# Optimization experiments

Hardware: AMD Instinct MI355X
Metric: run time of the kernel (lower is better)

Reference implementation:

```python
import jax, jax.numpy as jnp
import numpy as np

B, N, NB, P = 4, 2048, 10, 5
BIG = 1.0e5  # fill value for non-positive gt grasps


def _build_grasps(approach, base, contacts, thickness):
    # approach/base/contacts: [B,N,3], thickness: [B,N] -> [B,N,4,4]
    cross = jnp.cross(approach, base)
    R = jnp.stack([base, cross, approach], axis=-1)            # columns: [base, cross, approach]
    t = contacts + thickness[..., None] * 0.5 * base           # [B,N,3]
    top = jnp.concatenate([R, t[..., None]], axis=-1)          # [B,N,3,4]
    bottom = jnp.broadcast_to(jnp.array([0.0, 0.0, 0.0, 1.0], top.dtype),
                              top.shape[:-2] + (1, 4))
    return jnp.concatenate([top, bottom], axis=-2)             # [B,N,4,4]


def _transform_cps(cp_h, grasps):
    # cp_h: [P,4], grasps: [B,N,4,4] -> transformed control points [B,N,P,3]
    # torch: matmul(control_points, grasps^T)[..., :3]
    return jnp.einsum('pk,bnjk->bnpj', cp_h, grasps)[..., :3]


def _pairwise_sq(a, b):
    # a: [B,Na,P,3], b: [B,Nb,P,3] -> [B,Na,Nb] = sum_{p,c} (a-b)^2
    af = a.reshape(a.shape[0], a.shape[1], -1)
    bf = b.reshape(b.shape[0], b.shape[1], -1)
    a2 = jnp.sum(af * af, axis=-1)
    b2 = jnp.sum(bf * bf, axis=-1)
    d = a2[:, :, None] + b2[:, None, :] - 2.0 * jnp.einsum('bnd,bmd->bnm', af, bf)
    return jnp.maximum(d, 0.0)


def _forward(grasp_dir_head, approach_dir_head, grasp_offset_head, pred_points,
             binary_score_pred, binary_score_head, dir_labels_pc_cam, offset_labels_pc,
             grasp_success_labels_pc, approach_labels_pc_cam, bin_vals, bin_weights,
             control_pts, sym_control_pts):
    succ = grasp_success_labels_pc                              # [B,N] in {0,1}
    pos_in_view = jnp.maximum(jnp.sum(succ, axis=1), 1.0)       # min_geom_loss_divisor = 1.0

    # bin_offsets=True: lookup bin value of argmax bin
    thickness_pred = bin_vals[jnp.argmax(grasp_offset_head, axis=2)]   # [B,N]
    thickness_gt = bin_vals[jnp.argmax(offset_labels_pc, axis=2)]      # [B,N]

    pred_grasps = _build_grasps(approach_dir_head, grasp_dir_head, pred_points, thickness_pred)
    gt_grasps = _build_grasps(approach_labels_pc_cam, dir_labels_pc_cam, pred_points, thickness_gt)
    mask4 = succ.astype(bool)[:, :, None, None]
    pos_gt_grasps = jnp.where(mask4, gt_grasps, jnp.full_like(gt_grasps, BIG))

    ones_col = jnp.ones((P, 1), dtype=control_pts.dtype)
    cp_h = jnp.concatenate([control_pts, ones_col], axis=1)      # [P,4]
    scp_h = jnp.concatenate([sym_control_pts, ones_col], axis=1)

    pred_cp = _transform_cps(cp_h, pred_grasps)                  # [B,N,P,3]
    gt_cp_pos = _transform_cps(cp_h, pos_gt_grasps)
    sym_gt_cp_pos = _transform_cps(scp_h, pos_gt_grasps)

    # pred -> gt ADD-S (top-k with k=1 == min over concat of the two [B,N,N])
    d1 = _pairwise_sq(pred_cp, gt_cp_pos)
    d2 = _pairwise_sq(pred_cp, sym_gt_cp_pos)
    best = jnp.min(jnp.minimum(d1, d2), axis=2)                  # [B,N]
    gate = jnp.minimum(jnp.sum(succ, axis=1, keepdims=True), 1.0)
    min_adds = gate * jnp.sqrt(best)
    adds_loss = jnp.mean(binary_score_pred[:, :, 0] * min_adds)

    # gt -> pred ADD-S with unmasked gt grasps + confidence gather
    gt_cp = _transform_cps(cp_h, gt_grasps)
    sym_gt_cp = _transform_cps(scp_h, gt_grasps)
    dg1 = _pairwise_sq(gt_cp, pred_cp)                           # [B,Ngt,Npred]
    dg2 = _pairwise_sq(sym_gt_cp, pred_cp)
    m1 = jnp.min(dg1, axis=2); i1 = jnp.argmin(dg1, axis=2)
    m2 = jnp.min(dg2, axis=2); i2 = jnp.argmin(dg2, axis=2)
    # torch: where(-m1 < -m2, sym_idcs, idcs) == pick sym when m2 < m1
    idcs = jnp.where(m2 < m1, i2, i1)                            # [B,N]
    min_g2p = jnp.minimum(m1, m2) * succ
    conf = jnp.take_along_axis(binary_score_pred[:, :, 0], idcs, axis=1)
    adds_loss_gt2pred = jnp.mean(jnp.sum(conf * min_g2p, axis=1) / pos_in_view)

    # direction cosine loss
    cos_d = 1.0 - jnp.sum(dir_labels_pc_cam * grasp_dir_head, axis=2)
    dir_cosine_loss = jnp.mean(jnp.sum(cos_d * succ, axis=1) / pos_in_view)

    # approach cosine loss against orthogonalized label
    proj = jnp.sum(grasp_dir_head * approach_labels_pc_cam, axis=2, keepdims=True)
    orthog = approach_labels_pc_cam - proj * grasp_dir_head
    orthog = orthog / jnp.maximum(jnp.linalg.norm(orthog, axis=2, keepdims=True), 1e-12)
    cos_a = 1.0 - jnp.sum(orthog * approach_dir_head, axis=2)
    approach_cosine_loss = jnp.mean(jnp.sum(cos_a * succ, axis=1) / pos_in_view)

    # per-bin sigmoid BCE offset loss, bin-weighted
    bce = (offset_labels_pc * jax.nn.softplus(-grasp_offset_head)
           + (1.0 - offset_labels_pc) * jax.nn.softplus(grasp_offset_head))
    off = jnp.mean(bin_weights[None, None, :] * bce, axis=2)
    offset_loss = jnp.mean(jnp.sum(off * succ, axis=1) / pos_in_view)

    # binary success score BCE
    s = succ[:, :, None]
    score_bce = (s * jax.nn.softplus(-binary_score_head)
                 + (1.0 - s) * jax.nn.softplus(binary_score_head))
    bin_ce_loss = jnp.mean(score_bce)

    total = (1.0 * dir_cosine_loss + 1.0 * bin_ce_loss + 1.0 * offset_loss
             + 1.0 * approach_cosine_loss + 10.0 * adds_loss + 1.0 * adds_loss_gt2pred)
    return total


def setup_inputs():
    key = jax.random.key(0)
    ks = jax.random.split(key, 14)
    unit = lambda x: x / jnp.linalg.norm(x, axis=-1, keepdims=True)
    grasp_dir_head = unit(jax.random.normal(ks[0], (B, N, 3), jnp.float32))
    approach_dir_head = unit(jax.random.normal(ks[1], (B, N, 3), jnp.float32))
    grasp_offset_head = jax.random.normal(ks[2], (B, N, NB), jnp.float32)
    pred_points = jax.random.normal(ks[3], (B, N, 3), jnp.float32) * 0.3
    binary_score_pred = jax.random.uniform(ks[4], (B, N, 1), jnp.float32)
    binary_score_head = jax.random.normal(ks[5], (B, N, 1), jnp.float32)
    dir_labels_pc_cam = unit(jax.random.normal(ks[6], (B, N, 3), jnp.float32))
    offset_labels_pc = jax.nn.one_hot(jax.random.randint(ks[7], (B, N), 0, NB), NB, dtype=jnp.float32)
    grasp_success_labels_pc = jnp.round(jax.random.uniform(ks[8], (B, N), jnp.float32))
    approach_labels_pc_cam = unit(jax.random.normal(ks[9], (B, N, 3), jnp.float32))
    bin_vals = jnp.sort(jax.random.uniform(ks[10], (NB,), jnp.float32) * 0.075)
    bin_weights = jax.random.uniform(ks[11], (NB,), jnp.float32) + 0.5
    control_pts = jax.random.normal(ks[12], (P, 3), jnp.float32) * 0.05
    sym_control_pts = control_pts[jnp.array([0, 1, 3, 2, 4])]  # finger-swapped (symmetric) gripper
    return {
        'grasp_dir_head': grasp_dir_head,
        'approach_dir_head': approach_dir_head,
        'grasp_offset_head': grasp_offset_head,
        'pred_points': pred_points,
        'binary_score_pred': binary_score_pred,
        'binary_score_head': binary_score_head,
        'dir_labels_pc_cam': dir_labels_pc_cam,
        'offset_labels_pc': offset_labels_pc,
        'grasp_success_labels_pc': grasp_success_labels_pc,
        'approach_labels_pc_cam': approach_labels_pc_cam,
        'bin_vals': bin_vals,
        'bin_weights': bin_weights,
        'control_pts': control_pts,
        'sym_control_pts': sym_control_pts,
    }


def reference(grasp_dir_head, approach_dir_head, grasp_offset_head, pred_points,
              binary_score_pred, binary_score_head, dir_labels_pc_cam, offset_labels_pc,
              grasp_success_labels_pc, approach_labels_pc_cam, bin_vals, bin_weights,
              control_pts, sym_control_pts):
    return _forward(grasp_dir_head, approach_dir_head, grasp_offset_head, pred_points,
                    binary_score_pred, binary_score_head, dir_labels_pc_cam, offset_labels_pc,
                    grasp_success_labels_pc, approach_labels_pc_cam, bin_vals, bin_weights,
                    control_pts, sym_control_pts)
```

## Files before the change

### kernel.cpp

```cpp
#include <hip/hip_runtime.h>

#define Bn 4
#define Nn 2048
#define NBn 10
#define BN (Bn*Nn)
#define TCOLS 256
#define NCH 64
#define BIGM 1e32f

#define OFF_PRED 0
#define OFF_GT   (BN*16)
#define OFF_PN2  (2*BN*16)
#define OFF_GN2  (OFF_PN2 + BN)
#define OFF_BEST (OFF_GN2 + BN)
#define OFF_PK   (OFF_BEST + BN)
#define OFF_PART (OFF_PK + BN)

__device__ inline float sp_(float x) {
  return fmaxf(x, 0.0f) + log1pf(expf(-fabsf(x)));
}

__device__ inline float waveMin_(float v) {
  const int INFI = 0x7F800000;
#define DPPMIN(ctrl) \
  v = fminf(v, __int_as_float(__builtin_amdgcn_update_dpp(INFI, __float_as_int(v), ctrl, 0xf, 0xf, false)))
  DPPMIN(0x111);
  DPPMIN(0x112);
  DPPMIN(0x114);
  DPPMIN(0x118);
  DPPMIN(0x142);
  DPPMIN(0x143);
#undef DPPMIN
  return v;
}

__device__ inline float blockSum_(float v, float* red) {
  #pragma unroll
  for (int o = 32; o > 0; o >>= 1) v += __shfl_down(v, o, 64);
  __syncthreads();
  if ((threadIdx.x & 63) == 0) red[threadIdx.x >> 6] = v;
  __syncthreads();
  return red[0] + red[1] + red[2] + red[3];
}

__global__ __launch_bounds__(256) void k_prep(
    const float* __restrict__ gdir, const float* __restrict__ adirp,
    const float* __restrict__ goff, const float* __restrict__ ppts,
    const float* __restrict__ bsh,
    const float* __restrict__ dlab, const float* __restrict__ olab,
    const float* __restrict__ succ, const float* __restrict__ alab,
    const float* __restrict__ binv, const float* __restrict__ binw,
    const float* __restrict__ cpts, const float* __restrict__ scpts,
    float* __restrict__ ws)
{
  __shared__ float red[4];
  const int pb = blockIdx.x;
  const int idx = pb * 256 + threadIdx.x;

  const float gd0=gdir[idx*3+0],  gd1=gdir[idx*3+1],  gd2=gdir[idx*3+2];
  const float ad0=adirp[idx*3+0], ad1=adirp[idx*3+1], ad2=adirp[idx*3+2];
  const float dl0=dlab[idx*3+0],  dl1=dlab[idx*3+1],  dl2=dlab[idx*3+2];
  const float al0=alab[idx*3+0],  al1=alab[idx*3+1],  al2=alab[idx*3+2];
  const float pt0=ppts[idx*3+0],  pt1=ppts[idx*3+1],  pt2=ppts[idx*3+2];
  const float sc = succ[idx];

  float bv = goff[idx*NBn]; int ap = 0;
  #pragma unroll
  for (int k = 1; k < NBn; k++) { float v = goff[idx*NBn+k]; if (v > bv) { bv = v; ap = k; } }
  float bg = olab[idx*NBn]; int ag = 0;
  #pragma unroll
  for (int k = 1; k < NBn; k++) { float v = olab[idx*NBn+k]; if (v > bg) { bg = v; ag = k; } }
  const float tp = binv[ap] * 0.5f;
  const float tg = binv[ag] * 0.5f;

  const float cp0 = ad1*gd2 - ad2*gd1, cp1 = ad2*gd0 - ad0*gd2, cp2 = ad0*gd1 - ad1*gd0;
  const float cg0 = al1*dl2 - al2*dl1, cg1 = al2*dl0 - al0*dl2, cg2 = al0*dl1 - al1*dl0;
  const float tpx = pt0 + tp*gd0, tpy = pt1 + tp*gd1, tpz = pt2 + tp*gd2;
  const float tgx = pt0 + tg*dl0, tgy = pt1 + tg*dl1, tgz = pt2 + tg*dl2;

  float pcp[15], gcp[15];
  float pn2 = 0.f, gn2 = 0.f;
  #pragma unroll
  for (int p = 0; p < 5; p++) {
    const float cx = cpts[p*3], cy = cpts[p*3+1], cz = cpts[p*3+2];
    float x, y, z;
    x = gd0*cx + cp0*cy + ad0*cz + tpx;
    y = gd1*cx + cp1*cy + ad1*cz + tpy;
    z = gd2*cx + cp2*cy + ad2*cz + tpz;
    pcp[p*3+0]=x; pcp[p*3+1]=y; pcp[p*3+2]=z;
    pn2 = fmaf(x,x, fmaf(y,y, fmaf(z,z, pn2)));
    x = dl0*cx + cg0*cy + al0*cz + tgx;
    y = dl1*cx + cg1*cy + al1*cz + tgy;
    z = dl2*cx + cg2*cy + al2*cz + tgz;
    gcp[p*3+0]=x; gcp[p*3+1]=y; gcp[p*3+2]=z;
    gn2 = fmaf(x,x, fmaf(y,y, fmaf(z,z, gn2)));
  }

  float4* pd = (float4*)(ws + OFF_PRED) + (size_t)idx*4;
  pd[0]=make_float4(pcp[0],pcp[1],pcp[2],pcp[3]);
  pd[1]=make_float4(pcp[4],pcp[5],pcp[6],pcp[7]);
  pd[2]=make_float4(pcp[8],pcp[9],pcp[10],pcp[11]);
  pd[3]=make_float4(pcp[12],pcp[13],pcp[14],0.f);
  float4* gdst = (float4*)(ws + OFF_GT) + (size_t)idx*4;
  gdst[0]=make_float4(gcp[0],gcp[1],gcp[2],gcp[3]);
  gdst[1]=make_float4(gcp[4],gcp[5],gcp[6],gcp[7]);
  gdst[2]=make_float4(gcp[8],gcp[9],gcp[10],gcp[11]);
  gdst[3]=make_float4(gcp[12],gcp[13],gcp[14],0.f);
  ws[OFF_PN2+idx] = pn2; ws[OFF_GN2+idx] = gn2;

  ((unsigned*)ws)[OFF_BEST + idx] = 0x7F800000u;
  ((unsigned*)ws)[OFF_PK   + idx] = 0xFFFFFFFFu;

  const float cosd = 1.f - (dl0*gd0 + dl1*gd1 + dl2*gd2);
  const float proj = gd0*al0 + gd1*al1 + gd2*al2;
  const float o0 = al0 - proj*gd0, o1 = al1 - proj*gd1, o2 = al2 - proj*gd2;
  const float on = sqrtf(o0*o0 + o1*o1 + o2*o2);
  const float inv = 1.f / fmaxf(on, 1e-12f);
  const float cosa = 1.f - inv*(o0*ad0 + o1*ad1 + o2*ad2);

  float offv = 0.f;
  #pragma unroll
  for (int k = 0; k < NBn; k++) {
    const float x = goff[idx*NBn+k], lab = olab[idx*NBn+k];
    const float bce = lab * sp_(-x) + (1.f - lab) * sp_(x);
    offv = fmaf(binw[k], bce, offv);
  }
  offv *= (1.0f / NBn);
  const float sb = bsh[idx];
  const float sbce = sc * sp_(-sb) + (1.f - sc) * sp_(sb);

  float* part = ws + OFF_PART + (size_t)pb*8;
  float t;
  t = blockSum_(cosd*sc, red); if (threadIdx.x == 0) part[0] = t;
  t = blockSum_(cosa*sc, red); if (threadIdx.x == 0) part[1] = t;
  t = blockSum_(offv*sc, red); if (threadIdx.x == 0) part[2] = t;
  t = blockSum_(sc, red);      if (threadIdx.x == 0) part[3] = t;
  t = blockSum_(sbce, red);    if (threadIdx.x == 0) part[4] = t;
}

__global__ __launch_bounds__(256, 2) void k_pair(const float* __restrict__ succ,
                                                 float* __restrict__ ws) {
  __shared__ float pls[NCH*16];
  __shared__ float pn2s[NCH];
  __shared__ unsigned bkey[TCOLS];
  const int tile = blockIdx.x * TCOLS, b = blockIdx.z;
  const int bN = b * Nn;
  const int ny0 = blockIdx.y * NCH;
  const int tid = threadIdx.x;
  const int lane = tid & 63;
  const int wid = __builtin_amdgcn_readfirstlane(tid >> 6);

  {
    const int row = tid >> 2, q = tid & 3;
    ((float4*)pls)[tid] = ((const float4*)(ws + OFF_PRED))[(size_t)(bN + ny0 + row)*4 + q];
    if (tid < NCH) pn2s[tid] = ws[OFF_PN2 + bN + ny0 + tid];
    bkey[tid] = 0xFFFFFFFFu;
  }

  float4 gq[4][4];
  float  gnc[4], biasc[4], ex[4], ey[4], ez[4];
  unsigned kk[4];
  const float4* G = (const float4*)(ws + OFF_GT);
  #pragma unroll
  for (int c = 0; c < 4; c++) {
    const int r = bN + tile + c*64 + lane;
    gq[c][0] = G[(size_t)r*4+0]; gq[c][1] = G[(size_t)r*4+1];
    gq[c][2] = G[(size_t)r*4+2]; gq[c][3] = G[(size_t)r*4+3];
    gnc[c]   = ws[OFF_GN2 + r];
    biasc[c] = (succ[r] != 0.f) ? 0.f : BIGM;
    ex[c] = gq[c][2].y - gq[c][1].z;
    ey[c] = gq[c][2].z - gq[c][1].w;
    ez[c] = gq[c][2].w - gq[c][2].x;
    kk[c] = 0xFFFFFFFFu;
  }

  float f[16];
  __syncthreads();

  const float4* PL = (const float4*)pls + (size_t)wid*16*4;

  #pragma unroll
  for (int j = 0; j < 16; j++) {
    const float4 p0 = PL[j*4+0], p1 = PL[j*4+1], p2 = PL[j*4+2], p3 = PL[j*4+3];
    const float pn2 = pn2s[wid*16 + j];
    const float pd0 = p1.z - p2.y, pd1 = p1.w - p2.z, pd2 = p2.x - p2.w;
    const unsigned nl = (unsigned)(ny0 + wid*16 + j), nh = nl | 0x800u;

    float fj = BIGM * 2.f;
    #pragma unroll
    for (int c = 0; c < 4; c++) {
      float s;
      s = fmaf(p0.w, gq[c][0].w, fmaf(p0.z, gq[c][0].z, fmaf(p0.y, gq[c][0].y, p0.x*gq[c][0].x)));
      s = fmaf(p1.w, gq[c][1].w, fmaf(p1.z, gq[c][1].z, fmaf(p1.y, gq[c][1].y, fmaf(p1.x, gq[c][1].x, s))));
      s = fmaf(p2.w, gq[c][2].w, fmaf(p2.z, gq[c][2].z, fmaf(p2.y, gq[c][2].y, fmaf(p2.x, gq[c][2].x, s))));
      const float dot = fmaf(p3.z, gq[c][3].z, fmaf(p3.y, gq[c][3].y, fmaf(p3.x, gq[c][3].x, s)));
      const float del = fmaf(pd0, ex[c], fmaf(pd1, ey[c], pd2*ez[c]));
      const float q1  = fmaf(-2.f, dot, pn2 + gnc[c]);
      const float d1  = fmaxf(q1, 0.f);
      const float d2  = fmaxf(fmaf(-2.f, del, q1), 0.f);

      kk[c] = min(kk[c], min((__float_as_uint(d1) & 0xFFFFF000u) | nl,
                             (__float_as_uint(d2) & 0xFFFFF000u) | nh));

      fj = fminf(fj, fminf(d1, d2) + biasc[c]);
    }
    f[j] = fj;
  }

  #pragma unroll
  for (int j = 0; j < 16; j++) f[j] = waveMin_(f[j]);
  if (lane == 63) {
    #pragma unroll
    for (int j = 0; j < 16; j++)
      atomicMin((unsigned*)ws + OFF_BEST + bN + ny0 + wid*16 + j, __float_as_uint(f[j]));
  }

  #pragma unroll
  for (int c = 0; c < 4; c++) atomicMin(&bkey[c*64 + lane], kk[c]);
  __syncthreads();
  atomicMin((unsigned*)ws + OFF_PK + bN + tile + tid, bkey[tid]);
}

__global__ __launch_bounds__(256) void k_red(const float* __restrict__ bsp,
                                             const float* __restrict__ succ,
                                             float* __restrict__ ws) {
  __shared__ float red[4];
  const int b = blockIdx.y, nt = blockIdx.x;
  const int idx = b*Nn + nt*256 + threadIdx.x;

  const float best = __uint_as_float(((const unsigned*)ws)[OFF_BEST + idx]);
  const float adds = (best < 1e30f) ? bsp[idx] * sqrtf(best) : 0.f;

  const unsigned key = ((const unsigned*)ws)[OFF_PK + idx];
  const float d = __uint_as_float(key & 0xFFFFF000u);
  const int  id = (int)(key & 0x7FFu);
  const float g2p = bsp[b*Nn + id] * d * succ[idx];

  float* part = ws + OFF_PART + (size_t)(b*8 + nt)*8;
  float t;
  t = blockSum_(adds, red); if (threadIdx.x == 0) part[5] = t;
  t = blockSum_(g2p, red);  if (threadIdx.x == 0) part[6] = t;
}

__global__ __launch_bounds__(64) void k_fin(const float* __restrict__ ws, float* __restrict__ out) {
  const int t = threadIdx.x;
  float v[7];
  #pragma unroll
  for (int c = 0; c < 7; c++) v[c] = (t < 32) ? ws[OFF_PART + t*8 + c] : 0.f;
  #pragma unroll
  for (int o = 1; o < 8; o <<= 1) {
    #pragma unroll
    for (int c = 0; c < 7; c++) v[c] += __shfl_xor(v[c], o, 64);
  }
  const float pos = fmaxf(v[3], 1.f);
  float vb   = (v[0] + v[1] + v[2] + v[6]) / pos;
  float bce  = v[4];
  float adds = v[5];
  #pragma unroll
  for (int o = 8; o < 32; o <<= 1) {
    vb   += __shfl_xor(vb,   o, 64);
    bce  += __shfl_xor(bce,  o, 64);
    adds += __shfl_xor(adds, o, 64);
  }
  if (t == 0)
    out[0] = vb * 0.25f + bce * (1.f/BN) + 10.f * adds * (1.f/BN);
}

extern "C" void kernel_launch(void* const* d_in, const int* in_sizes, int n_in,
                              void* d_out, int out_size, void* d_ws, size_t ws_size,
                              hipStream_t stream) {
  const float* gdir  = (const float*)d_in[0];
  const float* adirp = (const float*)d_in[1];
  const float* goff  = (const float*)d_in[2];
  const float* ppts  = (const float*)d_in[3];
  const float* bsp   = (const float*)d_in[4];
  const float* bsh   = (const float*)d_in[5];
  const float* dlab  = (const float*)d_in[6];
  const float* olab  = (const float*)d_in[7];
  const float* succ  = (const float*)d_in[8];
  const float* alab  = (const float*)d_in[9];
  const float* binv  = (const float*)d_in[10];
  const float* binw  = (const float*)d_in[11];
  const float* cpts  = (const float*)d_in[12];
  const float* scpts = (const float*)d_in[13];
  float* ws  = (float*)d_ws;
  float* out = (float*)d_out;
  (void)scpts;

  k_prep<<<dim3(BN/256), dim3(256), 0, stream>>>(gdir, adirp, goff, ppts, bsh,
                                                 dlab, olab, succ, alab,
                                                 binv, binw, cpts, scpts, ws);
  k_pair<<<dim3(Nn/TCOLS, Nn/NCH, Bn), dim3(256), 0, stream>>>(succ, ws);
  k_red<<<dim3(Nn/256, Bn), dim3(256), 0, stream>>>(bsp, succ, ws);
  k_fin<<<1, 64, 0, stream>>>(ws, out);
}
```

Before: 116.5 us.

## Double pair-kernel rows per block and fuse final reduction into last-block pattern

Each k_pair block now processes 128 predicted rows instead of 64, in two passes of 16 rows per wave. This halves the block count and the number of per-column atomicMin flushes, and reuses the gt registers across more rows. The separate k_fin launch is merged into k_red through a global counter, so the last block to finish does the final reduction. That removes one kernel launch but adds a threadfence and an atomic, and relies on the counter being reset in k_prep.

```diff
diff --git a/kernel.cpp b/kernel.cpp
--- a/kernel.cpp
+++ b/kernel.cpp
@@ -5,7 +5,7 @@
 #define NBn 10
 #define BN (Bn*Nn)
 #define TCOLS 256
-#define NCH 64
+#define NCH 128
 #define BIGM 1e32f
 
 #define OFF_PRED 0
@@ -15,6 +15,7 @@
 #define OFF_BEST (OFF_GN2 + BN)
 #define OFF_PK   (OFF_BEST + BN)
 #define OFF_PART (OFF_PK + BN)
+#define OFF_CNT  (OFF_PART + 32*8)
 
 __device__ inline float sp_(float x) {
   return fmaxf(x, 0.0f) + log1pf(expf(-fabsf(x)));
@@ -110,6 +111,7 @@
 
   ((unsigned*)ws)[OFF_BEST + idx] = 0x7F800000u;
   ((unsigned*)ws)[OFF_PK   + idx] = 0xFFFFFFFFu;
+  if (idx == 0) ((unsigned*)ws)[OFF_CNT] = 0u;
 
   const float cosd = 1.f - (dl0*gd0 + dl1*gd1 + dl2*gd2);
   const float proj = gd0*al0 + gd1*al1 + gd2*al2;
@@ -151,8 +153,12 @@
   const int wid = __builtin_amdgcn_readfirstlane(tid >> 6);
 
   {
-    const int row = tid >> 2, q = tid & 3;
-    ((float4*)pls)[tid] = ((const float4*)(ws + OFF_PRED))[(size_t)(bN + ny0 + row)*4 + q];
+    #pragma unroll
+    for (int e = 0; e < 2; e++) {
+      const int ent = e*256 + tid;
+      const int row = ent >> 2, q = ent & 3;
+      ((float4*)pls)[ent] = ((const float4*)(ws + OFF_PRED))[(size_t)(bN + ny0 + row)*4 + q];
+    }
     if (tid < NCH) pn2s[tid] = ws[OFF_PN2 + bN + ny0 + tid];
     bkey[tid] = 0xFFFFFFFFu;
   }
@@ -173,46 +179,48 @@
     ez[c] = gq[c][2].w - gq[c][2].x;
     kk[c] = 0xFFFFFFFFu;
   }
-
-  float f[16];
-  __syncthreads();
-
-  const float4* PL = (const float4*)pls + (size_t)wid*16*4;
-
-  #pragma unroll
-  for (int j = 0; j < 16; j++) {
-    const float4 p0 = PL[j*4+0], p1 = PL[j*4+1], p2 = PL[j*4+2], p3 = PL[j*4+3];
-    const float pn2 = pn2s[wid*16 + j];
-    const float pd0 = p1.z - p2.y, pd1 = p1.w - p2.z, pd2 = p2.x - p2.w;
-    const unsigned nl = (unsigned)(ny0 + wid*16 + j), nh = nl | 0x800u;
-
-    float fj = BIGM * 2.f;
+  __syncthreads();
+
+  for (int p = 0; p < 2; p++) {
+    const int rbase = wid*32 + p*16;
+    const float4* PL = (const float4*)pls + (size_t)rbase*4;
+    float f[16];
+
     #pragma unroll
-    for (int c = 0; c < 4; c++) {
-      float s;
-      s = fmaf(p0.w, gq[c][0].w, fmaf(p0.z, gq[c][0].z, fmaf(p0.y, gq[c][0].y, p0.x*gq[c][0].x)));
-      s = fmaf(p1.w, gq[c][1].w, fmaf(p1.z, gq[c][1].z, fmaf(p1.y, gq[c][1].y, fmaf(p1.x, gq[c][1].x, s))));
-      s = fmaf(p2.w, gq[c][2].w, fmaf(p2.z, gq[c][2].z, fmaf(p2.y, gq[c][2].y, fmaf(p2.x, gq[c][2].x, s))));
-      const float dot = fmaf(p3.z, gq[c][3].z, fmaf(p3.y, gq[c][3].y, fmaf(p3.x, gq[c][3].x, s)));
-      const float del = fmaf(pd0, ex[c], fmaf(pd1, ey[c], pd2*ez[c]));
-      const float q1  = fmaf(-2.f, dot, pn2 + gnc[c]);
-      const float d1  = fmaxf(q1, 0.f);
-      const float d2  = fmaxf(fmaf(-2.f, del, q1), 0.f);
-
-      kk[c] = min(kk[c], min((__float_as_uint(d1) & 0xFFFFF000u) | nl,
-                             (__float_as_uint(d2) & 0xFFFFF000u) | nh));
-
-      fj = fminf(fj, fminf(d1, d2) + biasc[c]);
+    for (int j = 0; j < 16; j++) {
+      const float4 p0 = PL[j*4+0], p1 = PL[j*4+1], p2 = PL[j*4+2], p3 = PL[j*4+3];
+      const float pn2 = pn2s[rbase + j];
+      const float pd0 = p1.z - p2.y, pd1 = p1.w - p2.z, pd2 = p2.x - p2.w;
+      const unsigned nl = (unsigned)(ny0 + rbase + j), nh = nl | 0x800u;
+
+      float fj = BIGM * 2.f;
+      #pragma unroll
+      for (int c = 0; c < 4; c++) {
+        float s;
+        s = fmaf(p0.w, gq[c][0].w, fmaf(p0.z, gq[c][0].z, fmaf(p0.y, gq[c][0].y, p0.x*gq[c][0].x)));
+        s = fmaf(p1.w, gq[c][1].w, fmaf(p1.z, gq[c][1].z, fmaf(p1.y, gq[c][1].y, fmaf(p1.x, gq[c][1].x, s))));
+        s = fmaf(p2.w, gq[c][2].w, fmaf(p2.z, gq[c][2].z, fmaf(p2.y, gq[c][2].y, fmaf(p2.x, gq[c][2].x, s))));
+        const float dot = fmaf(p3.z, gq[c][3].z, fmaf(p3.y, gq[c][3].y, fmaf(p3.x, gq[c][3].x, s)));
+        const float del = fmaf(pd0, ex[c], fmaf(pd1, ey[c], pd2*ez[c]));
+        const float q1  = fmaf(-2.f, dot, pn2 + gnc[c]);
+        const float d1  = fmaxf(q1, 0.f);
+        const float d2  = fmaxf(fmaf(-2.f, del, q1), 0.f);
+
+        kk[c] = min(kk[c], min((__float_as_uint(d1) & 0xFFFFF000u) | nl,
+                               (__float_as_uint(d2) & 0xFFFFF000u) | nh));
+
+        fj = fminf(fj, fminf(d1, d2) + biasc[c]);
+      }
+      f[j] = fj;
     }
-    f[j] = fj;
-  }
-
-  #pragma unroll
-  for (int j = 0; j < 16; j++) f[j] = waveMin_(f[j]);
-  if (lane == 63) {
+
     #pragma unroll
-    for (int j = 0; j < 16; j++)
-      atomicMin((unsigned*)ws + OFF_BEST + bN + ny0 + wid*16 + j, __float_as_uint(f[j]));
+    for (int j = 0; j < 16; j++) f[j] = waveMin_(f[j]);
+    if (lane == 63) {
+      #pragma unroll
+      for (int j = 0; j < 16; j++)
+        atomicMin((unsigned*)ws + OFF_BEST + bN + ny0 + rbase + j, __float_as_uint(f[j]));
+    }
   }
 
   #pragma unroll
@@ -221,10 +229,12 @@
   atomicMin((unsigned*)ws + OFF_PK + bN + tile + tid, bkey[tid]);
 }
 
-__global__ __launch_bounds__(256) void k_red(const float* __restrict__ bsp,
-                                             const float* __restrict__ succ,
-                                             float* __restrict__ ws) {
+__global__ __launch_bounds__(256) void k_redfin(const float* __restrict__ bsp,
+                                                const float* __restrict__ succ,
+                                                float* __restrict__ ws,
+                                                float* __restrict__ out) {
   __shared__ float red[4];
+  __shared__ int isLast;
   const int b = blockIdx.y, nt = blockIdx.x;
   const int idx = b*Nn + nt*256 + threadIdx.x;
 
@@ -240,13 +250,19 @@
   float t;
   t = blockSum_(adds, red); if (threadIdx.x == 0) part[5] = t;
   t = blockSum_(g2p, red);  if (threadIdx.x == 0) part[6] = t;
-}
-
-__global__ __launch_bounds__(64) void k_fin(const float* __restrict__ ws, float* __restrict__ out) {
-  const int t = threadIdx.x;
+
+  __threadfence();
+  if (threadIdx.x == 0)
+    isLast = (atomicAdd((unsigned*)ws + OFF_CNT, 1u) == 31u);
+  __syncthreads();
+  if (!isLast) return;
+  __threadfence();
+
+  const int tt = threadIdx.x;
+  if (tt >= 64) return;
   float v[7];
   #pragma unroll
-  for (int c = 0; c < 7; c++) v[c] = (t < 32) ? ws[OFF_PART + t*8 + c] : 0.f;
+  for (int c = 0; c < 7; c++) v[c] = (tt < 32) ? ws[OFF_PART + tt*8 + c] : 0.f;
   #pragma unroll
   for (int o = 1; o < 8; o <<= 1) {
     #pragma unroll
@@ -255,15 +271,15 @@
   const float pos = fmaxf(v[3], 1.f);
   float vb   = (v[0] + v[1] + v[2] + v[6]) / pos;
   float bce  = v[4];
-  float adds = v[5];
+  float adds2 = v[5];
   #pragma unroll
   for (int o = 8; o < 32; o <<= 1) {
-    vb   += __shfl_xor(vb,   o, 64);
-    bce  += __shfl_xor(bce,  o, 64);
-    adds += __shfl_xor(adds, o, 64);
-  }
-  if (t == 0)
-    out[0] = vb * 0.25f + bce * (1.f/BN) + 10.f * adds * (1.f/BN);
+    vb    += __shfl_xor(vb,    o, 64);
+    bce   += __shfl_xor(bce,   o, 64);
+    adds2 += __shfl_xor(adds2, o, 64);
+  }
+  if (tt == 0)
+    out[0] = vb * 0.25f + bce * (1.f/BN) + 10.f * adds2 * (1.f/BN);
 }
 
 extern "C" void kernel_launch(void* const* d_in, const int* in_sizes, int n_in,
@@ -291,6 +307,5 @@
                                                  dlab, olab, succ, alab,
                                                  binv, binw, cpts, scpts, ws);
   k_pair<<<dim3(Nn/TCOLS, Nn/NCH, Bn), dim3(256), 0, stream>>>(succ, ws);
-  k_red<<<dim3(Nn/256, Bn), dim3(256), 0, stream>>>(bsp, succ, ws);
-  k_fin<<<1, 64, 0, stream>>>(ws, out);
-}
+  k_redfin<<<dim3(Nn/256, Bn), dim3(256), 0, stream>>>(bsp, succ, ws, out);
+}
```

New measurement: 114.9 us. Within noise of the previous version (-1.4%).
